# Performance work log

Measured on AMD Instinct MI355X. Metric: run time of the kernel, lower is better.

The kernel has to match this reference:

```python
import jax, jax.numpy as jnp
import numpy as np

N = 50000      # nodes
E = 800000     # edges (before self loops)
IN_DIM = 256
HID = 64       # per-head hidden dim
HEADS = 4
NEG_SLOPE = 0.2


def setup_inputs() -> dict:
    key = jax.random.key(0)
    k1, k2, k3, k4, k5, k6 = jax.random.split(key, 6)
    x = jax.random.normal(k1, (N, IN_DIM), dtype=jnp.float32)
    edge_index = jax.random.randint(k2, (2, E), 0, N, dtype=jnp.int64)
    # GATConv params (PyG layout): lin weight, att_src, att_dst, bias
    W = jax.random.normal(k3, (IN_DIM, HEADS * HID), dtype=jnp.float32) / np.sqrt(IN_DIM)
    att_src = jax.random.normal(k4, (HEADS, HID), dtype=jnp.float32) / np.sqrt(HID)
    att_dst = jax.random.normal(k5, (HEADS, HID), dtype=jnp.float32) / np.sqrt(HID)
    bias = jnp.zeros((HEADS * HID,), dtype=jnp.float32)
    return {"x": x, "edge_index": edge_index, "W": W,
            "att_src": att_src, "att_dst": att_dst, "bias": bias}


def _gat_forward(x, edge_index, W, att_src, att_dst, bias):
    n = x.shape[0]
    # linear projection per head: [N, H, F]
    h = (x @ W).reshape(n, HEADS, HID)
    # per-node attention logits (computed once on nodes, then gathered)
    a_src = jnp.einsum('nhf,hf->nh', h, att_src)  # [N, H]
    a_dst = jnp.einsum('nhf,hf->nh', h, att_dst)  # [N, H]
    # add self loops (PyG default add_self_loops=True)
    loop = jnp.arange(n, dtype=edge_index.dtype)
    src = jnp.concatenate([edge_index[0], loop])  # [E+N]
    dst = jnp.concatenate([edge_index[1], loop])  # [E+N]
    # edge attention logits with LeakyReLU
    e = jax.nn.leaky_relu(a_src[src] + a_dst[dst], NEG_SLOPE)  # [E+N, H]
    # segment softmax over incoming edges of each destination node
    m = jax.ops.segment_max(e, dst, num_segments=n)            # [N, H]
    num = jnp.exp(e - m[dst])                                  # [E+N, H]
    denom = jax.ops.segment_sum(num, dst, num_segments=n)      # [N, H]
    alpha = num / denom[dst]                                   # [E+N, H]
    # scatter-aggregate weighted source features
    msg = alpha[:, :, None] * h[src]                           # [E+N, H, F]
    out = jax.ops.segment_sum(msg, dst, num_segments=n)        # [N, H, F]
    out = out.reshape(n, HEADS * HID) + bias
    # GraphEncoder.forward: ReLU then Dropout (dropout=0 -> identity)
    return jax.nn.relu(out)


def reference(x, edge_index, W, att_src, att_dst, bias):
    return _gat_forward(x, edge_index, W, att_src, att_dst, bias)
```

## Files before the change

kernel.cpp:

```cpp
#include <hip/hip_runtime.h>
#include <hip/hip_bf16.h>

#define N_NODES 50000
#define N_EDGES 800000
#define TOT_EDGES (N_EDGES + N_NODES)
#define IN_DIM 256
#define OUT_DIM 256
#define HEADS 4
#define NEG_SLOPE 0.2f
#define CAP 96

#define FBLK 1024
#define GBLK 1563
#define LDS_STRIDE 264

typedef __bf16 bf16x8 __attribute__((ext_vector_type(8)));
typedef __bf16 bf16x4 __attribute__((ext_vector_type(4)));
typedef float f32x4 __attribute__((ext_vector_type(4)));

__device__ __forceinline__ float b2f(unsigned short u) {
    union { float f; unsigned int i; } v; v.i = ((unsigned int)u) << 16; return v.f;
}

__device__ __forceinline__ bool detect64(const int* __restrict__ ei, int t) {
    int nz = 0;
    for (int i = t; i < 1024; i += 256)
        if (ei[2 * i + 1] != 0) nz++;
    return __syncthreads_count(nz) == 0;
}

struct Args {
    const float* x; const int* ei; const float* W;
    const float* att_s; const float* att_d; const float* bias;
    float* out;
    __bf16* Wt; __bf16* h; float* a_src; float* a_dst;
    int* counts; int* ell;
};

__global__ void k_wt(Args A) {
    int k = blockIdx.x;
    int n = threadIdx.x;
    A.Wt[(size_t)n * IN_DIM + k] = (__bf16)A.W[(size_t)k * OUT_DIM + n];
    int idx = blockIdx.x * 256 + threadIdx.x;
    if (idx < N_NODES) A.counts[idx] = 0;
}

__global__ __launch_bounds__(256) void k_gemm_fill(Args A) {
    __shared__ __bf16 xs[32 * LDS_STRIDE];
    const int t = threadIdx.x;

    if (blockIdx.x >= FBLK) {
        const int mbase = (blockIdx.x - FBLK) * 32;
        const float4* x4 = (const float4*)A.x;
#pragma unroll
        for (int i = 0; i < 8; ++i) {
            int f = i * 256 + t;
            int row = f >> 6;
            int c4  = f & 63;
            int grow = mbase + row;
            if (grow >= N_NODES) grow = N_NODES - 1;
            float4 v = x4[(size_t)grow * 64 + c4];
            bf16x4 o = { (__bf16)v.x, (__bf16)v.y, (__bf16)v.z, (__bf16)v.w };
            *(bf16x4*)&xs[row * LDS_STRIDE + c4 * 4] = o;
        }
        __syncthreads();

        const int wave = t >> 6;
        const int lane = t & 63;
        const int cc   = lane & 15;
        const int quad = lane >> 4;
        const int n0   = wave * 64;
        f32x4 acc[2][4];
#pragma unroll
        for (int mt = 0; mt < 2; ++mt)
#pragma unroll
            for (int j = 0; j < 4; ++j) acc[mt][j] = (f32x4){0.f, 0.f, 0.f, 0.f};

        for (int k0 = 0; k0 < IN_DIM; k0 += 32) {
            bf16x8 b0 = *(const bf16x8*)(A.Wt + (size_t)(n0 + cc)      * IN_DIM + k0 + quad * 8);
            bf16x8 b1 = *(const bf16x8*)(A.Wt + (size_t)(n0 + 16 + cc) * IN_DIM + k0 + quad * 8);
            bf16x8 b2 = *(const bf16x8*)(A.Wt + (size_t)(n0 + 32 + cc) * IN_DIM + k0 + quad * 8);
            bf16x8 b3 = *(const bf16x8*)(A.Wt + (size_t)(n0 + 48 + cc) * IN_DIM + k0 + quad * 8);
#pragma unroll
            for (int mt = 0; mt < 2; ++mt) {
                bf16x8 a = *(const bf16x8*)&xs[(mt * 16 + cc) * LDS_STRIDE + k0 + quad * 8];
                acc[mt][0] = __builtin_amdgcn_mfma_f32_16x16x32_bf16(a, b0, acc[mt][0], 0, 0, 0);
                acc[mt][1] = __builtin_amdgcn_mfma_f32_16x16x32_bf16(a, b1, acc[mt][1], 0, 0, 0);
                acc[mt][2] = __builtin_amdgcn_mfma_f32_16x16x32_bf16(a, b2, acc[mt][2], 0, 0, 0);
                acc[mt][3] = __builtin_amdgcn_mfma_f32_16x16x32_bf16(a, b3, acc[mt][3], 0, 0, 0);
            }
        }

        float as0 = A.att_s[n0 + cc],      as1 = A.att_s[n0 + 16 + cc];
        float as2 = A.att_s[n0 + 32 + cc], as3 = A.att_s[n0 + 48 + cc];
        float ad0 = A.att_d[n0 + cc],      ad1 = A.att_d[n0 + 16 + cc];
        float ad2 = A.att_d[n0 + 32 + cc], ad3 = A.att_d[n0 + 48 + cc];
#pragma unroll
        for (int mt = 0; mt < 2; ++mt) {
#pragma unroll
            for (int r = 0; r < 4; ++r) {
                int row = mbase + mt * 16 + quad * 4 + r;
                float pS = acc[mt][0][r] * as0 + acc[mt][1][r] * as1
                         + acc[mt][2][r] * as2 + acc[mt][3][r] * as3;
                float pD = acc[mt][0][r] * ad0 + acc[mt][1][r] * ad1
                         + acc[mt][2][r] * ad2 + acc[mt][3][r] * ad3;
#pragma unroll
                for (int o = 8; o >= 1; o >>= 1) {
                    pS += __shfl_xor(pS, o, 64);
                    pD += __shfl_xor(pD, o, 64);
                }
                if (row < N_NODES && cc == 0) {
                    A.a_src[row * 4 + wave] = pS;
                    A.a_dst[row * 4 + wave] = pD;
                }
            }
        }

        __syncthreads();
#pragma unroll
        for (int mt = 0; mt < 2; ++mt)
#pragma unroll
            for (int j = 0; j < 4; ++j)
#pragma unroll
                for (int r = 0; r < 4; ++r)
                    xs[(mt * 16 + quad * 4 + r) * LDS_STRIDE + n0 + j * 16 + cc] =
                        (__bf16)acc[mt][j][r];
        __syncthreads();
#pragma unroll
        for (int i = 0; i < 4; ++i) {
            int idx = i * 256 + t;
            int row = idx >> 5;
            int c8  = idx & 31;
            int grow = mbase + row;
            if (grow < N_NODES)
                *(bf16x8*)(A.h + (size_t)grow * OUT_DIM + c8 * 8) =
                    *(const bf16x8*)&xs[row * LDS_STRIDE + c8 * 8];
        }
    } else {
        bool is64 = detect64(A.ei, t);
        const long long* ei64 = (const long long*)A.ei;
        for (int i = blockIdx.x * 256 + t; i < TOT_EDGES; i += FBLK * 256) {
            int s, d;
            if (i < N_EDGES) {
                if (is64) { s = (int)ei64[i]; d = (int)ei64[N_EDGES + i]; }
                else      { s = A.ei[i];      d = A.ei[N_EDGES + i]; }
            } else {
                s = d = i - N_EDGES;
            }
            int pos = atomicAdd(&A.counts[d], 1);
            if (pos < CAP) A.ell[(size_t)d * CAP + pos] = s;
        }
    }
}

__global__ __launch_bounds__(256) void k_agg(Args A) {
    __shared__ float lds_all[4][CAP][4];
    int wave = threadIdx.x >> 6, lane = threadIdx.x & 63;
    int node = blockIdx.x * 4 + wave;
    if (node >= N_NODES) return;
    float (*lds)[4] = lds_all[wave];

    int base = node * CAP;
    int deg  = A.counts[node];
    if (deg > CAP) deg = CAP;
    const float4* as4 = (const float4*)A.a_src;
    float4 ad = ((const float4*)A.a_dst)[node];

    float4 smv = {0.f, 0.f, 0.f, 0.f};
    for (int e = lane; e < deg; e += 64) {
        int s = A.ell[base + e];
        float4 av = as4[s];
        float4 l;
        l.x = av.x + ad.x; l.x = l.x > 0.f ? l.x : NEG_SLOPE * l.x;
        l.y = av.y + ad.y; l.y = l.y > 0.f ? l.y : NEG_SLOPE * l.y;
        l.z = av.z + ad.z; l.z = l.z > 0.f ? l.z : NEG_SLOPE * l.z;
        l.w = av.w + ad.w; l.w = l.w > 0.f ? l.w : NEG_SLOPE * l.w;
        float4 e4;
        e4.x = __expf(l.x); e4.y = __expf(l.y);
        e4.z = __expf(l.z); e4.w = __expf(l.w);
        smv.x += e4.x; smv.y += e4.y; smv.z += e4.z; smv.w += e4.w;
        lds[e][0] = e4.x; lds[e][1] = e4.y; lds[e][2] = e4.z; lds[e][3] = e4.w;
    }
    int padEnd = (deg + 3) & ~3;
    for (int e = deg + lane; e < padEnd; e += 64) {
        lds[e][0] = 0.f; lds[e][1] = 0.f; lds[e][2] = 0.f; lds[e][3] = 0.f;
    }
#pragma unroll
    for (int o = 32; o >= 1; o >>= 1) {
        smv.x += __shfl_xor(smv.x, o, 64);
        smv.y += __shfl_xor(smv.y, o, 64);
        smv.z += __shfl_xor(smv.z, o, 64);
        smv.w += __shfl_xor(smv.w, o, 64);
    }

    int head = lane >> 4;
    float smh = head == 0 ? smv.x : head == 1 ? smv.y : head == 2 ? smv.z : smv.w;
    float inv_d = 1.f / smh;

    float acc0 = 0.f, acc1 = 0.f, acc2 = 0.f, acc3 = 0.f;
    const unsigned short* hs = reinterpret_cast<const unsigned short*>(A.h);
    int rEnd = padEnd;
    for (int e = 0; e < rEnd; e += 4) {
        int s0 = A.ell[base + e];
        int s1 = A.ell[base + ((e + 1 < deg) ? e + 1 : 0)];
        int s2 = A.ell[base + ((e + 2 < deg) ? e + 2 : 0)];
        int s3 = A.ell[base + ((e + 3 < deg) ? e + 3 : 0)];
        float al0 = lds[e][head];
        float al1 = lds[e + 1][head];
        float al2 = lds[e + 2][head];
        float al3 = lds[e + 3][head];
        ushort4 h0 = *(const ushort4*)(hs + (size_t)s0 * OUT_DIM + lane * 4);
        ushort4 h1 = *(const ushort4*)(hs + (size_t)s1 * OUT_DIM + lane * 4);
        ushort4 h2 = *(const ushort4*)(hs + (size_t)s2 * OUT_DIM + lane * 4);
        ushort4 h3 = *(const ushort4*)(hs + (size_t)s3 * OUT_DIM + lane * 4);
        acc0 += al0 * b2f(h0.x) + al1 * b2f(h1.x) + al2 * b2f(h2.x) + al3 * b2f(h3.x);
        acc1 += al0 * b2f(h0.y) + al1 * b2f(h1.y) + al2 * b2f(h2.y) + al3 * b2f(h3.y);
        acc2 += al0 * b2f(h0.z) + al1 * b2f(h1.z) + al2 * b2f(h2.z) + al3 * b2f(h3.z);
        acc3 += al0 * b2f(h0.w) + al1 * b2f(h1.w) + al2 * b2f(h2.w) + al3 * b2f(h3.w);
    }

    float4 bv = ((const float4*)A.bias)[lane];
    float v0 = acc0 * inv_d + bv.x;
    float v1 = acc1 * inv_d + bv.y;
    float v2 = acc2 * inv_d + bv.z;
    float v3 = acc3 * inv_d + bv.w;
    float4 o4;
    o4.x = v0 > 0.f ? v0 : 0.f;
    o4.y = v1 > 0.f ? v1 : 0.f;
    o4.z = v2 > 0.f ? v2 : 0.f;
    o4.w = v3 > 0.f ? v3 : 0.f;
    ((float4*)A.out)[(size_t)node * 64 + lane] = o4;
}

extern "C" void kernel_launch(void* const* d_in, const int* in_sizes, int n_in,
                              void* d_out, int out_size, void* d_ws, size_t ws_size,
                              hipStream_t stream) {
    (void)out_size; (void)ws_size;
    const void* p_x = nullptr; const void* p_ei = nullptr; const void* p_W = nullptr;
    const void* p_small[3] = {nullptr, nullptr, nullptr}; int nsmall = 0;
    for (int i = 0; i < n_in; ++i) {
        switch (in_sizes[i]) {
            case N_NODES * IN_DIM:      p_x = d_in[i]; break;
            case 2 * N_EDGES:           p_ei = d_in[i]; break;
            case IN_DIM * OUT_DIM:      p_W = d_in[i]; break;
            case OUT_DIM:               if (nsmall < 3) p_small[nsmall++] = d_in[i]; break;
            default: break;
        }
    }
    if (!p_x)  p_x  = d_in[0];
    if (!p_ei) p_ei = d_in[1];
    if (!p_W)  p_W  = d_in[2];
    if (nsmall < 3) { p_small[0] = d_in[3]; p_small[1] = d_in[4]; p_small[2] = d_in[5]; }

    char* ws = (char*)d_ws;
    size_t off = 0;
    auto alloc = [&](size_t bytes) -> void* {
        void* p = ws + off;
        off = (off + bytes + 255) & ~(size_t)255;
        return p;
    };
    Args A;
    A.Wt      = (__bf16*)alloc((size_t)IN_DIM * OUT_DIM * 2);
    A.h       = (__bf16*)alloc((size_t)N_NODES * OUT_DIM * 2);
    A.a_src   = (float*)alloc((size_t)N_NODES * HEADS * 4);
    A.a_dst   = (float*)alloc((size_t)N_NODES * HEADS * 4);
    A.counts  = (int*)alloc((size_t)N_NODES * 4);
    A.ell     = (int*)alloc((size_t)N_NODES * CAP * 4);

    A.x     = (const float*)p_x;
    A.ei    = (const int*)p_ei;
    A.W     = (const float*)p_W;
    A.att_s = (const float*)p_small[0];
    A.att_d = (const float*)p_small[1];
    A.bias  = (const float*)p_small[2];
    A.out   = (float*)d_out;

    k_wt<<<dim3(IN_DIM), dim3(OUT_DIM), 0, stream>>>(A);
    k_gemm_fill<<<dim3(FBLK + GBLK), dim3(256), 0, stream>>>(A);
    k_agg<<<dim3((N_NODES + 3) / 4), dim3(256), 0, stream>>>(A);
}
```

Measured before the change: 266.0 us.

## Make GEMM blocks persistent with register-resident weights and prefetched x tiles

Rework the fused GEMM/ELL-fill kernel into 512-thread blocks. A fixed set of 768 GEMM blocks loops over 32-row tiles, keeps its slice of the bf16 weights in registers across tiles, and prefetches the next x tile into registers while computing the current one. Attention logits now go through LDS and are reduced across wave pairs, and the output is staged in a separate LDS buffer so the next tile can be written into xs at the same time. Fill blocks are cut to 256 and widened to 512 threads. The aim is to stop reloading W for every tile and to hide x load latency, at the cost of higher register pressure, an extra LDS buffer and fewer blocks.

```diff
diff --git a/kernel.cpp b/kernel.cpp
--- a/kernel.cpp
+++ b/kernel.cpp
@@ -10,8 +10,9 @@
 #define NEG_SLOPE 0.2f
 #define CAP 96
 
-#define FBLK 1024
-#define GBLK 1563
+#define FBLK 256
+#define NGB  768
+#define NT   1563
 #define LDS_STRIDE 264
 
 typedef __bf16 bf16x8 __attribute__((ext_vector_type(8)));
@@ -20,13 +21,6 @@
 
 __device__ __forceinline__ float b2f(unsigned short u) {
     union { float f; unsigned int i; } v; v.i = ((unsigned int)u) << 16; return v.f;
-}
-
-__device__ __forceinline__ bool detect64(const int* __restrict__ ei, int t) {
-    int nz = 0;
-    for (int i = t; i < 1024; i += 256)
-        if (ei[2 * i + 1] != 0) nz++;
-    return __syncthreads_count(nz) == 0;
 }
 
 struct Args {
@@ -45,101 +39,144 @@
     if (idx < N_NODES) A.counts[idx] = 0;
 }
 
-__global__ __launch_bounds__(256) void k_gemm_fill(Args A) {
+__global__ __launch_bounds__(512, 4) void k_gemm_fill(Args A) {
     __shared__ __bf16 xs[32 * LDS_STRIDE];
+    __shared__ __bf16 tr[32 * LDS_STRIDE];
+    __shared__ float  lg[2][8][32];
     const int t = threadIdx.x;
 
     if (blockIdx.x >= FBLK) {
-        const int mbase = (blockIdx.x - FBLK) * 32;
-        const float4* x4 = (const float4*)A.x;
-#pragma unroll
-        for (int i = 0; i < 8; ++i) {
-            int f = i * 256 + t;
-            int row = f >> 6;
-            int c4  = f & 63;
-            int grow = mbase + row;
-            if (grow >= N_NODES) grow = N_NODES - 1;
-            float4 v = x4[(size_t)grow * 64 + c4];
-            bf16x4 o = { (__bf16)v.x, (__bf16)v.y, (__bf16)v.z, (__bf16)v.w };
-            *(bf16x4*)&xs[row * LDS_STRIDE + c4 * 4] = o;
-        }
-        __syncthreads();
-
+        const int g    = blockIdx.x - FBLK;
         const int wave = t >> 6;
         const int lane = t & 63;
         const int cc   = lane & 15;
         const int quad = lane >> 4;
-        const int n0   = wave * 64;
-        f32x4 acc[2][4];
-#pragma unroll
-        for (int mt = 0; mt < 2; ++mt)
-#pragma unroll
-            for (int j = 0; j < 4; ++j) acc[mt][j] = (f32x4){0.f, 0.f, 0.f, 0.f};
-
-        for (int k0 = 0; k0 < IN_DIM; k0 += 32) {
-            bf16x8 b0 = *(const bf16x8*)(A.Wt + (size_t)(n0 + cc)      * IN_DIM + k0 + quad * 8);
-            bf16x8 b1 = *(const bf16x8*)(A.Wt + (size_t)(n0 + 16 + cc) * IN_DIM + k0 + quad * 8);
-            bf16x8 b2 = *(const bf16x8*)(A.Wt + (size_t)(n0 + 32 + cc) * IN_DIM + k0 + quad * 8);
-            bf16x8 b3 = *(const bf16x8*)(A.Wt + (size_t)(n0 + 48 + cc) * IN_DIM + k0 + quad * 8);
+        const int n0   = wave * 32;
+
+        bf16x8 Bf[8][2];
+#pragma unroll
+        for (int kk = 0; kk < 8; ++kk)
+#pragma unroll
+            for (int f = 0; f < 2; ++f)
+                Bf[kk][f] = *(const bf16x8*)(A.Wt
+                    + (size_t)(n0 + f * 16 + cc) * IN_DIM + kk * 32 + quad * 8);
+        float as0 = A.att_s[n0 + cc], as1 = A.att_s[n0 + 16 + cc];
+        float ad0 = A.att_d[n0 + cc], ad1 = A.att_d[n0 + 16 + cc];
+
+        const float4* x4 = (const float4*)A.x;
+
+        float4 st[4];
+#pragma unroll
+        for (int i = 0; i < 4; ++i) {
+            int f = i * 512 + t;
+            int row = f >> 6, c4 = f & 63;
+            int grow = g * 32 + row; if (grow >= N_NODES) grow = N_NODES - 1;
+            st[i] = x4[(size_t)grow * 64 + c4];
+        }
+#pragma unroll
+        for (int i = 0; i < 4; ++i) {
+            int f = i * 512 + t;
+            int row = f >> 6, c4 = f & 63;
+            bf16x4 o = { (__bf16)st[i].x, (__bf16)st[i].y, (__bf16)st[i].z, (__bf16)st[i].w };
+            *(bf16x4*)&xs[row * LDS_STRIDE + c4 * 4] = o;
+        }
+        __syncthreads();
+
+        for (int tile = g; tile < NT; tile += NGB) {
+            const int next = tile + NGB;
+            const bool hn = next < NT;
+            float4 st2[4];
+            if (hn) {
+#pragma unroll
+                for (int i = 0; i < 4; ++i) {
+                    int f = i * 512 + t;
+                    int row = f >> 6, c4 = f & 63;
+                    int grow = next * 32 + row; if (grow >= N_NODES) grow = N_NODES - 1;
+                    st2[i] = x4[(size_t)grow * 64 + c4];
+                }
+            }
+
+            f32x4 acc[2][2];
+#pragma unroll
+            for (int mt = 0; mt < 2; ++mt)
+#pragma unroll
+                for (int f = 0; f < 2; ++f) acc[mt][f] = (f32x4){0.f, 0.f, 0.f, 0.f};
+#pragma unroll
+            for (int kk = 0; kk < 8; ++kk) {
+#pragma unroll
+                for (int mt = 0; mt < 2; ++mt) {
+                    bf16x8 a = *(const bf16x8*)&xs[(mt * 16 + cc) * LDS_STRIDE + kk * 32 + quad * 8];
+                    acc[mt][0] = __builtin_amdgcn_mfma_f32_16x16x32_bf16(a, Bf[kk][0], acc[mt][0], 0, 0, 0);
+                    acc[mt][1] = __builtin_amdgcn_mfma_f32_16x16x32_bf16(a, Bf[kk][1], acc[mt][1], 0, 0, 0);
+                }
+            }
+
 #pragma unroll
             for (int mt = 0; mt < 2; ++mt) {
-                bf16x8 a = *(const bf16x8*)&xs[(mt * 16 + cc) * LDS_STRIDE + k0 + quad * 8];
-                acc[mt][0] = __builtin_amdgcn_mfma_f32_16x16x32_bf16(a, b0, acc[mt][0], 0, 0, 0);
-                acc[mt][1] = __builtin_amdgcn_mfma_f32_16x16x32_bf16(a, b1, acc[mt][1], 0, 0, 0);
-                acc[mt][2] = __builtin_amdgcn_mfma_f32_16x16x32_bf16(a, b2, acc[mt][2], 0, 0, 0);
-                acc[mt][3] = __builtin_amdgcn_mfma_f32_16x16x32_bf16(a, b3, acc[mt][3], 0, 0, 0);
-            }
-        }
-
-        float as0 = A.att_s[n0 + cc],      as1 = A.att_s[n0 + 16 + cc];
-        float as2 = A.att_s[n0 + 32 + cc], as3 = A.att_s[n0 + 48 + cc];
-        float ad0 = A.att_d[n0 + cc],      ad1 = A.att_d[n0 + 16 + cc];
-        float ad2 = A.att_d[n0 + 32 + cc], ad3 = A.att_d[n0 + 48 + cc];
-#pragma unroll
-        for (int mt = 0; mt < 2; ++mt) {
-#pragma unroll
-            for (int r = 0; r < 4; ++r) {
-                int row = mbase + mt * 16 + quad * 4 + r;
-                float pS = acc[mt][0][r] * as0 + acc[mt][1][r] * as1
-                         + acc[mt][2][r] * as2 + acc[mt][3][r] * as3;
-                float pD = acc[mt][0][r] * ad0 + acc[mt][1][r] * ad1
-                         + acc[mt][2][r] * ad2 + acc[mt][3][r] * ad3;
-#pragma unroll
-                for (int o = 8; o >= 1; o >>= 1) {
-                    pS += __shfl_xor(pS, o, 64);
-                    pD += __shfl_xor(pD, o, 64);
-                }
-                if (row < N_NODES && cc == 0) {
-                    A.a_src[row * 4 + wave] = pS;
-                    A.a_dst[row * 4 + wave] = pD;
-                }
-            }
-        }
-
-        __syncthreads();
-#pragma unroll
-        for (int mt = 0; mt < 2; ++mt)
-#pragma unroll
-            for (int j = 0; j < 4; ++j)
-#pragma unroll
-                for (int r = 0; r < 4; ++r)
-                    xs[(mt * 16 + quad * 4 + r) * LDS_STRIDE + n0 + j * 16 + cc] =
-                        (__bf16)acc[mt][j][r];
-        __syncthreads();
-#pragma unroll
-        for (int i = 0; i < 4; ++i) {
-            int idx = i * 256 + t;
-            int row = idx >> 5;
-            int c8  = idx & 31;
-            int grow = mbase + row;
-            if (grow < N_NODES)
-                *(bf16x8*)(A.h + (size_t)grow * OUT_DIM + c8 * 8) =
-                    *(const bf16x8*)&xs[row * LDS_STRIDE + c8 * 8];
+#pragma unroll
+                for (int r = 0; r < 4; ++r) {
+                    float pS = acc[mt][0][r] * as0 + acc[mt][1][r] * as1;
+                    float pD = acc[mt][0][r] * ad0 + acc[mt][1][r] * ad1;
+#pragma unroll
+                    for (int o = 8; o >= 1; o >>= 1) {
+                        pS += __shfl_xor(pS, o, 64);
+                        pD += __shfl_xor(pD, o, 64);
+                    }
+                    if (cc == 0) {
+                        lg[0][wave][mt * 16 + quad * 4 + r] = pS;
+                        lg[1][wave][mt * 16 + quad * 4 + r] = pD;
+                    }
+                }
+            }
+            __syncthreads();
+
+            if (hn) {
+#pragma unroll
+                for (int i = 0; i < 4; ++i) {
+                    int f = i * 512 + t;
+                    int row = f >> 6, c4 = f & 63;
+                    bf16x4 o = { (__bf16)st2[i].x, (__bf16)st2[i].y, (__bf16)st2[i].z, (__bf16)st2[i].w };
+                    *(bf16x4*)&xs[row * LDS_STRIDE + c4 * 4] = o;
+                }
+            }
+#pragma unroll
+            for (int mt = 0; mt < 2; ++mt)
+#pragma unroll
+                for (int f = 0; f < 2; ++f)
+#pragma unroll
+                    for (int r = 0; r < 4; ++r)
+                        tr[(mt * 16 + quad * 4 + r) * LDS_STRIDE + n0 + f * 16 + cc] =
+                            (__bf16)acc[mt][f][r];
+            if (t < 256) {
+                int td = t & 127;
+                int row = td >> 2, head = td & 3;
+                int grow = tile * 32 + row;
+                if (grow < N_NODES) {
+                    int sd = t >> 7;
+                    float v = lg[sd][2 * head][row] + lg[sd][2 * head + 1][row];
+                    float* dst = sd == 0 ? A.a_src : A.a_dst;
+                    dst[grow * 4 + head] = v;
+                }
+            }
+            __syncthreads();
+
+#pragma unroll
+            for (int i = 0; i < 2; ++i) {
+                int idx = i * 512 + t;
+                int row = idx >> 5, c8 = idx & 31;
+                int grow = tile * 32 + row;
+                if (grow < N_NODES)
+                    *(bf16x8*)(A.h + (size_t)grow * OUT_DIM + c8 * 8) =
+                        *(const bf16x8*)&tr[row * LDS_STRIDE + c8 * 8];
+            }
         }
     } else {
-        bool is64 = detect64(A.ei, t);
+        int nz = 0;
+        for (int i = t; i < 1024; i += 512)
+            if (A.ei[2 * i + 1] != 0) nz++;
+        bool is64 = (__syncthreads_count(nz) == 0);
         const long long* ei64 = (const long long*)A.ei;
-        for (int i = blockIdx.x * 256 + t; i < TOT_EDGES; i += FBLK * 256) {
+        for (int i = blockIdx.x * 512 + t; i < TOT_EDGES; i += FBLK * 512) {
             int s, d;
             if (i < N_EDGES) {
                 if (is64) { s = (int)ei64[i]; d = (int)ei64[N_EDGES + i]; }
@@ -276,6 +313,6 @@
     A.out   = (float*)d_out;
 
     k_wt<<<dim3(IN_DIM), dim3(OUT_DIM), 0, stream>>>(A);
-    k_gemm_fill<<<dim3(FBLK + GBLK), dim3(256), 0, stream>>>(A);
+    k_gemm_fill<<<dim3(FBLK + NGB), dim3(512), 0, stream>>>(A);
     k_agg<<<dim3((N_NODES + 3) / 4), dim3(256), 0, stream>>>(A);
 }
```

After: 246.1 us. -7.5%, faster.

## Split fused GEMM/fill kernel, enlarge GEMM row tile to 64, nontemporal output stores

Applied to the files above, without the earlier changes.

The combined GEMM+ELL-fill kernel is split into two launches: an edge-fill kernel with one thread per edge and a GEMM kernel whose row tile grows from 32 to 64, so each Wt fragment load feeds twice as many MFMAs. The counts array is now cleared with hipMemsetAsync instead of inside k_wt, and the final output uses nontemporal stores. The trade-off is one more kernel launch, the loss of overlap between fill and GEMM inside a single grid, and more registers and LDS per GEMM block, which may reduce occupancy.

```diff
diff --git a/kernel.cpp b/kernel.cpp
--- a/kernel.cpp
+++ b/kernel.cpp
@@ -10,8 +10,7 @@
 #define NEG_SLOPE 0.2f
 #define CAP 96
 
-#define FBLK 1024
-#define GBLK 1563
+#define GBLK 782
 #define LDS_STRIDE 264
 
 typedef __bf16 bf16x8 __attribute__((ext_vector_type(8)));
@@ -41,115 +40,115 @@
     int k = blockIdx.x;
     int n = threadIdx.x;
     A.Wt[(size_t)n * IN_DIM + k] = (__bf16)A.W[(size_t)k * OUT_DIM + n];
-    int idx = blockIdx.x * 256 + threadIdx.x;
-    if (idx < N_NODES) A.counts[idx] = 0;
-}
-
-__global__ __launch_bounds__(256) void k_gemm_fill(Args A) {
-    __shared__ __bf16 xs[32 * LDS_STRIDE];
+}
+
+__global__ __launch_bounds__(256) void k_fill(Args A) {
+    bool is64 = detect64(A.ei, threadIdx.x);
+    int i = blockIdx.x * 256 + threadIdx.x;
+    const long long* ei64 = (const long long*)A.ei;
+    if (i < N_EDGES) {
+        int s, d;
+        if (is64) { s = (int)ei64[i]; d = (int)ei64[N_EDGES + i]; }
+        else      { s = A.ei[i];      d = A.ei[N_EDGES + i]; }
+        int pos = atomicAdd(&A.counts[d], 1);
+        if (pos < CAP) A.ell[(size_t)d * CAP + pos] = s;
+    } else if (i < TOT_EDGES) {
+        int n = i - N_EDGES;
+        int pos = atomicAdd(&A.counts[n], 1);
+        if (pos < CAP) A.ell[(size_t)n * CAP + pos] = n;
+    }
+}
+
+__global__ __launch_bounds__(256) void k_gemm(Args A) {
+    __shared__ __bf16 xs[64 * LDS_STRIDE];
     const int t = threadIdx.x;
-
-    if (blockIdx.x >= FBLK) {
-        const int mbase = (blockIdx.x - FBLK) * 32;
-        const float4* x4 = (const float4*)A.x;
-#pragma unroll
-        for (int i = 0; i < 8; ++i) {
-            int f = i * 256 + t;
-            int row = f >> 6;
-            int c4  = f & 63;
-            int grow = mbase + row;
-            if (grow >= N_NODES) grow = N_NODES - 1;
-            float4 v = x4[(size_t)grow * 64 + c4];
-            bf16x4 o = { (__bf16)v.x, (__bf16)v.y, (__bf16)v.z, (__bf16)v.w };
-            *(bf16x4*)&xs[row * LDS_STRIDE + c4 * 4] = o;
+    const int mbase = blockIdx.x * 64;
+    const float4* __restrict__ x4 = (const float4*)A.x;
+    const __bf16* __restrict__ Wt = A.Wt;
+
+#pragma unroll
+    for (int i = 0; i < 16; ++i) {
+        int f = i * 256 + t;
+        int row = f >> 6;
+        int c4  = f & 63;
+        int grow = mbase + row;
+        if (grow >= N_NODES) grow = N_NODES - 1;
+        float4 v = x4[(size_t)grow * 64 + c4];
+        bf16x4 o = { (__bf16)v.x, (__bf16)v.y, (__bf16)v.z, (__bf16)v.w };
+        *(bf16x4*)&xs[row * LDS_STRIDE + c4 * 4] = o;
+    }
+    __syncthreads();
+
+    const int wave = t >> 6;
+    const int lane = t & 63;
+    const int cc   = lane & 15;
+    const int quad = lane >> 4;
+    const int n0   = wave * 64;
+    f32x4 acc[4][4];
+#pragma unroll
+    for (int mt = 0; mt < 4; ++mt)
+#pragma unroll
+        for (int j = 0; j < 4; ++j) acc[mt][j] = (f32x4){0.f, 0.f, 0.f, 0.f};
+
+    for (int k0 = 0; k0 < IN_DIM; k0 += 32) {
+        bf16x8 b0 = *(const bf16x8*)(Wt + (size_t)(n0 + cc)      * IN_DIM + k0 + quad * 8);
+        bf16x8 b1 = *(const bf16x8*)(Wt + (size_t)(n0 + 16 + cc) * IN_DIM + k0 + quad * 8);
+        bf16x8 b2 = *(const bf16x8*)(Wt + (size_t)(n0 + 32 + cc) * IN_DIM + k0 + quad * 8);
+        bf16x8 b3 = *(const bf16x8*)(Wt + (size_t)(n0 + 48 + cc) * IN_DIM + k0 + quad * 8);
+#pragma unroll
+        for (int mt = 0; mt < 4; ++mt) {
+            bf16x8 a = *(const bf16x8*)&xs[(mt * 16 + cc) * LDS_STRIDE + k0 + quad * 8];
+            acc[mt][0] = __builtin_amdgcn_mfma_f32_16x16x32_bf16(a, b0, acc[mt][0], 0, 0, 0);
+            acc[mt][1] = __builtin_amdgcn_mfma_f32_16x16x32_bf16(a, b1, acc[mt][1], 0, 0, 0);
+            acc[mt][2] = __builtin_amdgcn_mfma_f32_16x16x32_bf16(a, b2, acc[mt][2], 0, 0, 0);
+            acc[mt][3] = __builtin_amdgcn_mfma_f32_16x16x32_bf16(a, b3, acc[mt][3], 0, 0, 0);
         }
-        __syncthreads();
-
-        const int wave = t >> 6;
-        const int lane = t & 63;
-        const int cc   = lane & 15;
-        const int quad = lane >> 4;
-        const int n0   = wave * 64;
-        f32x4 acc[2][4];
-#pragma unroll
-        for (int mt = 0; mt < 2; ++mt)
-#pragma unroll
-            for (int j = 0; j < 4; ++j) acc[mt][j] = (f32x4){0.f, 0.f, 0.f, 0.f};
-
-        for (int k0 = 0; k0 < IN_DIM; k0 += 32) {
-            bf16x8 b0 = *(const bf16x8*)(A.Wt + (size_t)(n0 + cc)      * IN_DIM + k0 + quad * 8);
-            bf16x8 b1 = *(const bf16x8*)(A.Wt + (size_t)(n0 + 16 + cc) * IN_DIM + k0 + quad * 8);
-            bf16x8 b2 = *(const bf16x8*)(A.Wt + (size_t)(n0 + 32 + cc) * IN_DIM + k0 + quad * 8);
-            bf16x8 b3 = *(const bf16x8*)(A.Wt + (size_t)(n0 + 48 + cc) * IN_DIM + k0 + quad * 8);
-#pragma unroll
-            for (int mt = 0; mt < 2; ++mt) {
-                bf16x8 a = *(const bf16x8*)&xs[(mt * 16 + cc) * LDS_STRIDE + k0 + quad * 8];
-                acc[mt][0] = __builtin_amdgcn_mfma_f32_16x16x32_bf16(a, b0, acc[mt][0], 0, 0, 0);
-                acc[mt][1] = __builtin_amdgcn_mfma_f32_16x16x32_bf16(a, b1, acc[mt][1], 0, 0, 0);
-                acc[mt][2] = __builtin_amdgcn_mfma_f32_16x16x32_bf16(a, b2, acc[mt][2], 0, 0, 0);
-                acc[mt][3] = __builtin_amdgcn_mfma_f32_16x16x32_bf16(a, b3, acc[mt][3], 0, 0, 0);
+    }
+
+    float as0 = A.att_s[n0 + cc],      as1 = A.att_s[n0 + 16 + cc];
+    float as2 = A.att_s[n0 + 32 + cc], as3 = A.att_s[n0 + 48 + cc];
+    float ad0 = A.att_d[n0 + cc],      ad1 = A.att_d[n0 + 16 + cc];
+    float ad2 = A.att_d[n0 + 32 + cc], ad3 = A.att_d[n0 + 48 + cc];
+#pragma unroll
+    for (int mt = 0; mt < 4; ++mt) {
+#pragma unroll
+        for (int r = 0; r < 4; ++r) {
+            int row = mbase + mt * 16 + quad * 4 + r;
+            float pS = acc[mt][0][r] * as0 + acc[mt][1][r] * as1
+                     + acc[mt][2][r] * as2 + acc[mt][3][r] * as3;
+            float pD = acc[mt][0][r] * ad0 + acc[mt][1][r] * ad1
+                     + acc[mt][2][r] * ad2 + acc[mt][3][r] * ad3;
+#pragma unroll
+            for (int o = 8; o >= 1; o >>= 1) {
+                pS += __shfl_xor(pS, o, 64);
+                pD += __shfl_xor(pD, o, 64);
+            }
+            if (row < N_NODES && cc == 0) {
+                A.a_src[row * 4 + wave] = pS;
+                A.a_dst[row * 4 + wave] = pD;
             }
         }
-
-        float as0 = A.att_s[n0 + cc],      as1 = A.att_s[n0 + 16 + cc];
-        float as2 = A.att_s[n0 + 32 + cc], as3 = A.att_s[n0 + 48 + cc];
-        float ad0 = A.att_d[n0 + cc],      ad1 = A.att_d[n0 + 16 + cc];
-        float ad2 = A.att_d[n0 + 32 + cc], ad3 = A.att_d[n0 + 48 + cc];
-#pragma unroll
-        for (int mt = 0; mt < 2; ++mt) {
-#pragma unroll
-            for (int r = 0; r < 4; ++r) {
-                int row = mbase + mt * 16 + quad * 4 + r;
-                float pS = acc[mt][0][r] * as0 + acc[mt][1][r] * as1
-                         + acc[mt][2][r] * as2 + acc[mt][3][r] * as3;
-                float pD = acc[mt][0][r] * ad0 + acc[mt][1][r] * ad1
-                         + acc[mt][2][r] * ad2 + acc[mt][3][r] * ad3;
-#pragma unroll
-                for (int o = 8; o >= 1; o >>= 1) {
-                    pS += __shfl_xor(pS, o, 64);
-                    pD += __shfl_xor(pD, o, 64);
-                }
-                if (row < N_NODES && cc == 0) {
-                    A.a_src[row * 4 + wave] = pS;
-                    A.a_dst[row * 4 + wave] = pD;
-                }
-            }
-        }
-
-        __syncthreads();
-#pragma unroll
-        for (int mt = 0; mt < 2; ++mt)
-#pragma unroll
-            for (int j = 0; j < 4; ++j)
-#pragma unroll
-                for (int r = 0; r < 4; ++r)
-                    xs[(mt * 16 + quad * 4 + r) * LDS_STRIDE + n0 + j * 16 + cc] =
-                        (__bf16)acc[mt][j][r];
-        __syncthreads();
-#pragma unroll
-        for (int i = 0; i < 4; ++i) {
-            int idx = i * 256 + t;
-            int row = idx >> 5;
-            int c8  = idx & 31;
-            int grow = mbase + row;
-            if (grow < N_NODES)
-                *(bf16x8*)(A.h + (size_t)grow * OUT_DIM + c8 * 8) =
-                    *(const bf16x8*)&xs[row * LDS_STRIDE + c8 * 8];
-        }
-    } else {
-        bool is64 = detect64(A.ei, t);
-        const long long* ei64 = (const long long*)A.ei;
-        for (int i = blockIdx.x * 256 + t; i < TOT_EDGES; i += FBLK * 256) {
-            int s, d;
-            if (i < N_EDGES) {
-                if (is64) { s = (int)ei64[i]; d = (int)ei64[N_EDGES + i]; }
-                else      { s = A.ei[i];      d = A.ei[N_EDGES + i]; }
-            } else {
-                s = d = i - N_EDGES;
-            }
-            int pos = atomicAdd(&A.counts[d], 1);
-            if (pos < CAP) A.ell[(size_t)d * CAP + pos] = s;
-        }
+    }
+
+    __syncthreads();
+#pragma unroll
+    for (int mt = 0; mt < 4; ++mt)
+#pragma unroll
+        for (int j = 0; j < 4; ++j)
+#pragma unroll
+            for (int r = 0; r < 4; ++r)
+                xs[(mt * 16 + quad * 4 + r) * LDS_STRIDE + n0 + j * 16 + cc] =
+                    (__bf16)acc[mt][j][r];
+    __syncthreads();
+#pragma unroll
+    for (int i = 0; i < 8; ++i) {
+        int idx = i * 256 + t;
+        int row = idx >> 5;
+        int c8  = idx & 31;
+        int grow = mbase + row;
+        if (grow < N_NODES)
+            *(bf16x8*)(A.h + (size_t)grow * OUT_DIM + c8 * 8) =
+                *(const bf16x8*)&xs[row * LDS_STRIDE + c8 * 8];
     }
 }
 
@@ -220,16 +219,16 @@
     }
 
     float4 bv = ((const float4*)A.bias)[lane];
+    f32x4 o4;
     float v0 = acc0 * inv_d + bv.x;
     float v1 = acc1 * inv_d + bv.y;
     float v2 = acc2 * inv_d + bv.z;
     float v3 = acc3 * inv_d + bv.w;
-    float4 o4;
-    o4.x = v0 > 0.f ? v0 : 0.f;
-    o4.y = v1 > 0.f ? v1 : 0.f;
-    o4.z = v2 > 0.f ? v2 : 0.f;
-    o4.w = v3 > 0.f ? v3 : 0.f;
-    ((float4*)A.out)[(size_t)node * 64 + lane] = o4;
+    o4[0] = v0 > 0.f ? v0 : 0.f;
+    o4[1] = v1 > 0.f ? v1 : 0.f;
+    o4[2] = v2 > 0.f ? v2 : 0.f;
+    o4[3] = v3 > 0.f ? v3 : 0.f;
+    __builtin_nontemporal_store(o4, (f32x4*)A.out + (size_t)node * 64 + lane);
 }
 
 extern "C" void kernel_launch(void* const* d_in, const int* in_sizes, int n_in,
@@ -275,7 +274,9 @@
     A.bias  = (const float*)p_small[2];
     A.out   = (float*)d_out;
 
+    hipMemsetAsync(A.counts, 0, (size_t)N_NODES * 4, stream);
     k_wt<<<dim3(IN_DIM), dim3(OUT_DIM), 0, stream>>>(A);
-    k_gemm_fill<<<dim3(FBLK + GBLK), dim3(256), 0, stream>>>(A);
+    k_fill<<<dim3((TOT_EDGES + 255) / 256), dim3(256), 0, stream>>>(A);
+    k_gemm<<<dim3(GBLK), dim3(256), 0, stream>>>(A);
     k_agg<<<dim3((N_NODES + 3) / 4), dim3(256), 0, stream>>>(A);
 }
```

Result: no change. 263.3 us (-1.0%).
